# Kernel tuning notes

Measured on AMD Instinct MI355X. Metric: run time of the kernel, lower is better.

The kernel has to match this reference:

```python
import jax, jax.numpy as jnp
import numpy as np

# Transformer_E (depth=1): Residual(PreNorm(MultiScaleRetention)) + Residual1(PreNorm1(FeedForward))
# MultiScaleRetention follows the standard RetNet parallel form, adapted to two inputs
# (Q from x, K/V from z) as implied by PreNorm passing both normed streams to fn.

B, S, DIM, HEADS, MLP = 16, 1024, 256, 4, 512
HEAD = DIM // HEADS  # per-head qkv size; v_dim = DIM
EPS = 1e-5           # torch LayerNorm/GroupNorm default eps


def _ln(x, w, b):
    mu = jnp.mean(x, -1, keepdims=True)
    var = jnp.mean((x - mu) ** 2, -1, keepdims=True)
    return (x - mu) * jax.lax.rsqrt(var + EPS) * w + b


def _decay_matrix():
    # RetNet gammas: 1 - exp(linspace(log(1/32), log(1/512), heads))
    gammas = 1.0 - jnp.exp(jnp.linspace(jnp.log(1.0 / 32.0), jnp.log(1.0 / 512.0), HEADS))
    n = jnp.arange(S)
    diff = (n[:, None] - n[None, :]).astype(jnp.float32)  # [S,S]
    causal = diff >= 0
    D = jnp.where(causal[None], gammas[:, None, None] ** diff[None], 0.0)  # [H,S,S]
    return D.astype(jnp.float32)


def setup_inputs() -> dict:
    key = jax.random.key(0)
    ks = jax.random.split(key, 9)
    s = 1.0 / DIM  # repo inits W as randn/hidden_size
    return {
        "x": jax.random.normal(ks[0], (B, S, DIM), jnp.float32),
        "y": jax.random.normal(ks[1], (B, S, DIM), jnp.float32),
        "ln1_w": jnp.ones((DIM,), jnp.float32),
        "ln1_b": jnp.zeros((DIM,), jnp.float32),
        "W_Q": jax.random.normal(ks[2], (HEADS, DIM, HEAD), jnp.float32) * s,
        "W_K": jax.random.normal(ks[3], (HEADS, DIM, HEAD), jnp.float32) * s,
        "W_V": jax.random.normal(ks[4], (HEADS, DIM, HEAD), jnp.float32) * s,
        "gn_w": jnp.ones((DIM,), jnp.float32),
        "gn_b": jnp.zeros((DIM,), jnp.float32),
        "W_G": jax.random.normal(ks[5], (DIM, DIM), jnp.float32) * s,
        "W_O": jax.random.normal(ks[6], (DIM, DIM), jnp.float32) * s,
        "ln2_w": jnp.ones((DIM,), jnp.float32),
        "ln2_b": jnp.zeros((DIM,), jnp.float32),
        "ff_w1": jax.random.normal(ks[7], (DIM, MLP), jnp.float32) * (DIM ** -0.5),
        "ff_b1": jnp.zeros((MLP,), jnp.float32),
        "ff_w2": jax.random.normal(ks[8], (MLP, DIM), jnp.float32) * (MLP ** -0.5),
        "ff_b2": jnp.zeros((DIM,), jnp.float32),
    }


def reference(x, y, ln1_w, ln1_b, W_Q, W_K, W_V, gn_w, gn_b, W_G, W_O,
              ln2_w, ln2_b, ff_w1, ff_b1, ff_w2, ff_b2):
    # PreNorm: x.real -> float (already real float32 here), shared LayerNorm on both streams
    xn = _ln(x, ln1_w, ln1_b)
    zn = _ln(y, ln1_w, ln1_b)

    # --- MultiScaleRetention (parallel form) ---
    Q = jnp.einsum('bsd,hde->bhse', xn, W_Q)
    K = jnp.einsum('bsd,hde->bhse', zn, W_K)
    V = jnp.einsum('bsd,hde->bhse', zn, W_V)
    D = _decay_matrix()                                       # [H,S,S] causal decay
    scores = jnp.einsum('bhne,bhme->bhnm', Q, K) * D[None]    # [B,H,S,S]
    Yh = jnp.einsum('bhnm,bhme->bhne', scores, V)             # [B,H,S,HEAD]

    # GroupNorm(heads, v_dim) applied token-wise: normalize each head slice
    mu = jnp.mean(Yh, -1, keepdims=True)
    var = jnp.mean((Yh - mu) ** 2, -1, keepdims=True)
    Yn = (Yh - mu) * jax.lax.rsqrt(var + EPS)
    Ycat = jnp.transpose(Yn, (0, 2, 1, 3)).reshape(x.shape[0], x.shape[1], DIM)
    Ycat = Ycat * gn_w + gn_b

    # swish gate + output projection
    g = xn @ W_G
    attn_out = ((g * jax.nn.sigmoid(g)) * Ycat) @ W_O

    x1 = attn_out + x                                         # Residual

    # --- FeedForward block (Residual1(PreNorm1(FFN))) ---
    x1n = _ln(x1, ln2_w, ln2_b)
    h = jax.nn.leaky_relu(x1n @ ff_w1 + ff_b1, negative_slope=0.01)
    ff = h @ ff_w2 + ff_b2
    return ff + x1
```

## Files before the change

kernel.cpp:

```cpp
#include <hip/hip_runtime.h>

typedef float f32x4 __attribute__((ext_vector_type(4)));
typedef short bf16x8 __attribute__((ext_vector_type(8)));

__device__ __forceinline__ unsigned short f2bf(float f) {
  unsigned int u = __builtin_bit_cast(unsigned int, f);
  u += 0x7fffu + ((u >> 16) & 1u);
  return (unsigned short)(u >> 16);
}
__device__ __forceinline__ float bf2f(unsigned short s) {
  unsigned int u = ((unsigned int)s) << 16;
  return __builtin_bit_cast(float, u);
}

__device__ __forceinline__ void gll16(const void* src, void* dst) {
  __builtin_amdgcn_global_load_lds((const __attribute__((address_space(1))) void*)src,
                                   (__attribute__((address_space(3))) void*)dst, 16, 0, 0);
}

__global__ __launch_bounds__(256) void prep(
    const float* __restrict__ x, const float* __restrict__ y,
    const float* __restrict__ ln1w, const float* __restrict__ ln1b,
    const float* __restrict__ WQ, const float* __restrict__ WK,
    const float* __restrict__ WV, const float* __restrict__ WG,
    const float* __restrict__ WO, const float* __restrict__ F1,
    const float* __restrict__ F2,
    unsigned short* __restrict__ XN, unsigned short* __restrict__ ZN,
    unsigned short* __restrict__ qg, unsigned short* __restrict__ kv,
    unsigned short* __restrict__ wo, unsigned short* __restrict__ f1,
    unsigned short* __restrict__ f2)
{
  const int id = blockIdx.x;
  if (id < 8192) {
    const float* X = (id < 4096) ? x : y;
    unsigned short* Y = (id < 4096) ? XN : ZN;
    const int bid = id & 4095;
    const int lane = threadIdx.x & 63;
    const size_t row = (size_t)bid * 4 + (threadIdx.x >> 6);
    const float4 v = *reinterpret_cast<const float4*>(X + row * 256 + lane * 4);
    float s = v.x + v.y + v.z + v.w;
    #pragma unroll
    for (int off = 1; off < 64; off <<= 1) s += __shfl_xor(s, off);
    float mean = s * (1.0f / 256.0f);
    float dx = v.x - mean, dy = v.y - mean, dz = v.z - mean, dw = v.w - mean;
    float q = dx * dx + dy * dy + dz * dz + dw * dw;
    #pragma unroll
    for (int off = 1; off < 64; off <<= 1) q += __shfl_xor(q, off);
    float rstd = rsqrtf(q * (1.0f / 256.0f) + 1e-5f);
    float4 wv = *reinterpret_cast<const float4*>(ln1w + lane * 4);
    float4 bv = *reinterpret_cast<const float4*>(ln1b + lane * 4);
    ushort4 o;
    o.x = f2bf(dx * rstd * wv.x + bv.x);
    o.y = f2bf(dy * rstd * wv.y + bv.y);
    o.z = f2bf(dz * rstd * wv.z + bv.z);
    o.w = f2bf(dw * rstd * wv.w + bv.w);
    *reinterpret_cast<ushort4*>(Y + row * 256 + lane * 4) = o;
    return;
  }
  int i = (id - 8192) * 256 + threadIdx.x;
  if (i < 131072) {
    int n = i >> 8, d = i & 255;
    float v = (n < 256) ? WQ[((n >> 6) * 256 + d) * 64 + (n & 63)]
                        : WG[d * 256 + (n - 256)];
    qg[i] = f2bf(v);
  } else if (i < 262144) {
    int j = i - 131072; int n = j >> 8, d = j & 255;
    float v = (n < 256) ? WK[((n >> 6) * 256 + d) * 64 + (n & 63)]
                        : WV[(((n - 256) >> 6) * 256 + d) * 64 + ((n - 256) & 63)];
    kv[j] = f2bf(v);
  } else if (i < 327680) {
    int j = i - 262144; int n = j >> 8, d = j & 255;
    wo[j] = f2bf(WO[d * 256 + n]);
  } else if (i < 458752) {
    int j = i - 327680; int n = j >> 8, d = j & 255;
    f1[j] = f2bf(F1[d * 512 + n]);
  } else if (i < 589824) {
    int j = i - 458752; int n = j >> 9, k = j & 511;
    f2[j] = f2bf(F2[k * 256 + n]);
  }
}

__global__ __launch_bounds__(256) void gemm_qkvg(
    const unsigned short* __restrict__ XN, const unsigned short* __restrict__ ZN,
    const unsigned short* __restrict__ WQG, const unsigned short* __restrict__ WKV,
    unsigned short* __restrict__ QB, unsigned short* __restrict__ GB,
    unsigned short* __restrict__ KB, unsigned short* __restrict__ VT)
{
  __shared__ __align__(16) char sA[2][16384];
  __shared__ __align__(16) char sB[2][8192];
  const int tid = threadIdx.x, lane = tid & 63, w = tid >> 6;
  const int z = blockIdx.z;
  const unsigned short* A = z ? ZN : XN;
  const unsigned short* Bw = z ? WKV : WQG;
  const int flat = blockIdx.x + 8 * blockIdx.y;
  const int c = flat & 7, jj = flat >> 3;
  const int m0 = (c * 16 + (jj & 15)) * 128;
  const int n0 = (jj >> 4) * 64;
  const int wr = (w >> 1) * 64, wc = (w & 1) * 32;
  const char* Ab = (const char*)A + (size_t)m0 * 512;
  const char* Bb = (const char*)Bw + (size_t)n0 * 512;
  const int srow = lane >> 3;
  const int soff = 16 * ((lane & 7) ^ srow);
  f32x4 acc[4][2] = {};

  auto stage = [&](int bufi, int kt) {
    #pragma unroll
    for (int p = 0; p < 4; ++p) {
      int row = p * 32 + w * 8 + srow;
      gll16(Ab + (size_t)row * 512 + kt + soff, &sA[bufi][p * 4096 + w * 1024]);
    }
    #pragma unroll
    for (int p = 0; p < 2; ++p) {
      int row = p * 32 + w * 8 + srow;
      gll16(Bb + (size_t)row * 512 + kt + soff, &sB[bufi][p * 4096 + w * 1024]);
    }
  };

  stage(0, 0);
  asm volatile("s_waitcnt vmcnt(0)" ::: "memory");
  __syncthreads();
  int buf = 0;
  for (int kt = 0; kt < 512; kt += 128) {
    if (kt + 128 < 512) stage(buf ^ 1, kt + 128);
    #pragma unroll
    for (int kk = 0; kk < 2; ++kk) {
      const int ib = kk * 64 + ((lane >> 4) * 16);
      bf16x8 af[4], bfr[2];
      #pragma unroll
      for (int rf = 0; rf < 4; ++rf) {
        int row = wr + rf * 16 + (lane & 15);
        af[rf] = *reinterpret_cast<const bf16x8*>(&sA[buf][row * 128 + (ib ^ ((row & 7) << 4))]);
      }
      #pragma unroll
      for (int cf = 0; cf < 2; ++cf) {
        int row = wc + cf * 16 + (lane & 15);
        bfr[cf] = *reinterpret_cast<const bf16x8*>(&sB[buf][row * 128 + (ib ^ ((row & 7) << 4))]);
      }
      #pragma unroll
      for (int rf = 0; rf < 4; ++rf)
        #pragma unroll
        for (int cf = 0; cf < 2; ++cf)
          acc[rf][cf] = __builtin_amdgcn_mfma_f32_16x16x32_bf16(af[rf], bfr[cf], acc[rf][cf], 0, 0, 0);
    }
    asm volatile("s_waitcnt vmcnt(0)" ::: "memory");
    __syncthreads();
    buf ^= 1;
  }

  #pragma unroll
  for (int rf = 0; rf < 4; ++rf) {
    #pragma unroll
    for (int cf = 0; cf < 2; ++cf) {
      const int r0 = m0 + wr + rf * 16 + ((lane >> 4) * 4);
      const int col = n0 + wc + cf * 16 + (lane & 15);
      f32x4 v = acc[rf][cf];
      if (z == 0) {
        unsigned short* dst = (n0 < 256) ? QB : GB;
        int ccol = col & 255;
        #pragma unroll
        for (int j = 0; j < 4; ++j) dst[(size_t)(r0 + j) * 256 + ccol] = f2bf(v[j]);
      } else {
        if (n0 < 256) {
          #pragma unroll
          for (int j = 0; j < 4; ++j) KB[(size_t)(r0 + j) * 256 + col] = f2bf(v[j]);
        } else {
          int vc = col - 256, hh = vc >> 6, e = vc & 63;
          int bh = (r0 >> 10) * 4 + hh, s0 = r0 & 1023;
          ushort4 pk;
          pk.x = f2bf(v[0]); pk.y = f2bf(v[1]); pk.z = f2bf(v[2]); pk.w = f2bf(v[3]);
          *reinterpret_cast<ushort4*>(VT + (((size_t)bh * 64 + e) << 10) + s0) = pk;
        }
      }
    }
  }
}

template<int EPI>
__global__ __launch_bounds__(256) void gemm_nt(
    const unsigned short* __restrict__ A, const unsigned short* __restrict__ Bw,
    int K, unsigned short* __restrict__ o0,
    const float* __restrict__ bias, const float* __restrict__ resid,
    float* __restrict__ of)
{
  __shared__ __align__(16) char sA[2][16384];
  __shared__ __align__(16) char sB[2][8192];
  const int tid = threadIdx.x, lane = tid & 63, w = tid >> 6;
  const int flat = blockIdx.x + gridDim.x * blockIdx.y;
  const int c = flat & 7, jj = flat >> 3;
  const int m0 = (c * 16 + (jj & 15)) * 128;
  const int n0 = (jj >> 4) * 64;
  const int wr = (w >> 1) * 64, wc = (w & 1) * 32;
  const int K2 = K * 2;
  const char* Ab = (const char*)A + (size_t)m0 * K2;
  const char* Bb = (const char*)Bw + (size_t)n0 * K2;
  const int srow = lane >> 3;
  const int soff = 16 * ((lane & 7) ^ srow);
  f32x4 acc[4][2] = {};

  auto stage = [&](int bufi, int kt) {
    #pragma unroll
    for (int p = 0; p < 4; ++p) {
      int row = p * 32 + w * 8 + srow;
      gll16(Ab + (size_t)row * K2 + kt + soff, &sA[bufi][p * 4096 + w * 1024]);
    }
    #pragma unroll
    for (int p = 0; p < 2; ++p) {
      int row = p * 32 + w * 8 + srow;
      gll16(Bb + (size_t)row * K2 + kt + soff, &sB[bufi][p * 4096 + w * 1024]);
    }
  };

  stage(0, 0);
  asm volatile("s_waitcnt vmcnt(0)" ::: "memory");
  __syncthreads();
  int buf = 0;
  for (int kt = 0; kt < K2; kt += 128) {
    if (kt + 128 < K2) stage(buf ^ 1, kt + 128);
    #pragma unroll
    for (int kk = 0; kk < 2; ++kk) {
      const int ib = kk * 64 + ((lane >> 4) * 16);
      bf16x8 af[4], bfr[2];
      #pragma unroll
      for (int rf = 0; rf < 4; ++rf) {
        int row = wr + rf * 16 + (lane & 15);
        af[rf] = *reinterpret_cast<const bf16x8*>(&sA[buf][row * 128 + (ib ^ ((row & 7) << 4))]);
      }
      #pragma unroll
      for (int cf = 0; cf < 2; ++cf) {
        int row = wc + cf * 16 + (lane & 15);
        bfr[cf] = *reinterpret_cast<const bf16x8*>(&sB[buf][row * 128 + (ib ^ ((row & 7) << 4))]);
      }
      #pragma unroll
      for (int rf = 0; rf < 4; ++rf)
        #pragma unroll
        for (int cf = 0; cf < 2; ++cf)
          acc[rf][cf] = __builtin_amdgcn_mfma_f32_16x16x32_bf16(af[rf], bfr[cf], acc[rf][cf], 0, 0, 0);
    }
    asm volatile("s_waitcnt vmcnt(0)" ::: "memory");
    __syncthreads();
    buf ^= 1;
  }

  #pragma unroll
  for (int rf = 0; rf < 4; ++rf) {
    #pragma unroll
    for (int cf = 0; cf < 2; ++cf) {
      const int r0 = m0 + wr + rf * 16 + ((lane >> 4) * 4);
      const int col = n0 + wc + cf * 16 + (lane & 15);
      f32x4 v = acc[rf][cf];
      if constexpr (EPI == 3) {
        float bc = bias[col];
        #pragma unroll
        for (int j = 0; j < 4; ++j) {
          float t = v[j] + bc;
          o0[(size_t)(r0 + j) * 512 + col] = f2bf(t >= 0.0f ? t : 0.01f * t);
        }
      } else {
        float bc = bias[col];
        #pragma unroll
        for (int j = 0; j < 4; ++j) {
          size_t idx = (size_t)(r0 + j) * 256 + col;
          of[idx] = v[j] + bc + resid[idx];
        }
      }
    }
  }
}

__global__ __launch_bounds__(256) void gemm_wo_ln(
    const unsigned short* __restrict__ AY, const unsigned short* __restrict__ WoT,
    const float* __restrict__ x, const float* __restrict__ ln2w,
    const float* __restrict__ ln2b,
    float* __restrict__ X1, unsigned short* __restrict__ X1N)
{
  __shared__ __align__(16) char sA[2][4096];
  __shared__ __align__(16) char sB[2][32768];
  __shared__ float redS[32][4], redQ[32][4];
  const int tid = threadIdx.x, lane = tid & 63, w = tid >> 6;
  const int id = blockIdx.x;
  const int c = id & 7, j5 = id >> 3;
  const int m0 = (c * 64 + j5) * 32;
  const char* Ab = (const char*)AY + (size_t)m0 * 512;
  const char* Bb = (const char*)WoT;
  const int srow = lane >> 3;
  const int soff = 16 * ((lane & 7) ^ srow);
  f32x4 acc[2][4] = {};

  auto stage = [&](int bufi, int kt) {
    {
      int row = w * 8 + srow;
      gll16(Ab + (size_t)row * 512 + kt + soff, &sA[bufi][w * 1024]);
    }
    #pragma unroll
    for (int p = 0; p < 8; ++p) {
      int row = w * 64 + p * 8 + srow;
      gll16(Bb + (size_t)row * 512 + kt + soff, &sB[bufi][w * 8192 + p * 1024]);
    }
  };

  stage(0, 0);
  asm volatile("s_waitcnt vmcnt(0)" ::: "memory");
  __syncthreads();
  int buf = 0;
  for (int kt = 0; kt < 512; kt += 128) {
    if (kt + 128 < 512) stage(buf ^ 1, kt + 128);
    #pragma unroll
    for (int kk = 0; kk < 2; ++kk) {
      const int ib = kk * 64 + ((lane >> 4) * 16);
      bf16x8 af[2], bfr[4];
      #pragma unroll
      for (int mf = 0; mf < 2; ++mf) {
        int row = mf * 16 + (lane & 15);
        af[mf] = *reinterpret_cast<const bf16x8*>(&sA[buf][row * 128 + (ib ^ ((row & 7) << 4))]);
      }
      #pragma unroll
      for (int nf = 0; nf < 4; ++nf) {
        int row = w * 64 + nf * 16 + (lane & 15);
        bfr[nf] = *reinterpret_cast<const bf16x8*>(&sB[buf][row * 128 + (ib ^ ((row & 7) << 4))]);
      }
      #pragma unroll
      for (int mf = 0; mf < 2; ++mf)
        #pragma unroll
        for (int nf = 0; nf < 4; ++nf)
          acc[mf][nf] = __builtin_amdgcn_mfma_f32_16x16x32_bf16(af[mf], bfr[nf], acc[mf][nf], 0, 0, 0);
    }
    asm volatile("s_waitcnt vmcnt(0)" ::: "memory");
    __syncthreads();
    buf ^= 1;
  }

  #pragma unroll
  for (int mf = 0; mf < 2; ++mf) {
    #pragma unroll
    for (int j = 0; j < 4; ++j) {
      const int rowg = m0 + mf * 16 + ((lane >> 4) * 4) + j;
      float s = 0.0f, q = 0.0f;
      #pragma unroll
      for (int nf = 0; nf < 4; ++nf) {
        const int col = w * 64 + nf * 16 + (lane & 15);
        float v = acc[mf][nf][j] + x[(size_t)rowg * 256 + col];
        acc[mf][nf][j] = v;
        s += v; q += v * v;
      }
      #pragma unroll
      for (int off = 1; off < 16; off <<= 1) { s += __shfl_xor(s, off); q += __shfl_xor(q, off); }
      if ((lane & 15) == 0) {
        int rl = mf * 16 + ((lane >> 4) * 4) + j;
        redS[rl][w] = s; redQ[rl][w] = q;
      }
    }
  }
  __syncthreads();
  #pragma unroll
  for (int mf = 0; mf < 2; ++mf) {
    #pragma unroll
    for (int j = 0; j < 4; ++j) {
      const int rl = mf * 16 + ((lane >> 4) * 4) + j;
      const int rowg = m0 + rl;
      float sm = redS[rl][0] + redS[rl][1] + redS[rl][2] + redS[rl][3];
      float sq = redQ[rl][0] + redQ[rl][1] + redQ[rl][2] + redQ[rl][3];
      float mean = sm * (1.0f / 256.0f);
      float var = sq * (1.0f / 256.0f) - mean * mean;
      float rstd = rsqrtf(var + 1e-5f);
      #pragma unroll
      for (int nf = 0; nf < 4; ++nf) {
        const int col = w * 64 + nf * 16 + (lane & 15);
        float v = acc[mf][nf][j];
        X1[(size_t)rowg * 256 + col] = v;
        X1N[(size_t)rowg * 256 + col] = f2bf((v - mean) * rstd * ln2w[col] + ln2b[col]);
      }
    }
  }
}

__global__ __launch_bounds__(256) void attn_ret(
    const unsigned short* __restrict__ Qb, const unsigned short* __restrict__ Kb,
    const unsigned short* __restrict__ Vt, const unsigned short* __restrict__ Gb,
    const float* __restrict__ gnw, const float* __restrict__ gnb,
    unsigned short* __restrict__ AY)
{
  __shared__ __align__(16) char sK[2][8192];
  __shared__ __align__(16) char sV[2][8192];
  __shared__ __align__(16) char sP[8192];
  const int tid = threadIdx.x, lane = tid & 63, w = tid >> 6;
  const int id = blockIdx.x;
  const int c = id & 7, jid = id >> 3;
  const int bh = c * 8 + (jid & 7);
  const int g = jid >> 3;
  const int qt = (g < 4) ? (15 - g) : (g < 8) ? (11 - g) : (g < 12) ? g : (g - 12);
  const int b = bh >> 2, h = bh & 3;

  const float la = logf(1.0f / 32.0f), lb = logf(1.0f / 512.0f);
  const float gamma = 1.0f - expf(la + (lb - la) * ((float)h * (1.0f / 3.0f)));
  const float lg = log2f(gamma);

  const char* Qg = (const char*)Qb
      + ((size_t)(b * 1024 + qt * 64 + w * 16 + (lane & 15))) * 512 + h * 128 + (lane >> 4) * 16;
  const bf16x8 aq0 = *reinterpret_cast<const bf16x8*>(Qg);
  const bf16x8 aq1 = *reinterpret_cast<const bf16x8*>(Qg + 64);

  const int nloc_b = w * 16 + ((lane >> 4) * 4);
  float Aj[4], Bcf[4];
  #pragma unroll
  for (int j = 0; j < 4; ++j) Aj[j] = exp2f((float)(qt * 64 + nloc_b + j) * lg);
  #pragma unroll
  for (int cf = 0; cf < 4; ++cf) Bcf[cf] = exp2f(-(float)(cf * 16 + (lane & 15)) * lg);
  const float g64 = exp2f(-64.0f * lg);

  const char* Kg = (const char*)Kb + ((size_t)(b * 1024)) * 512 + h * 128;
  const char* Vg = (const char*)Vt + ((size_t)bh * 64) * 2048;
  const int srow = lane >> 3;
  const int soff = 16 * ((lane & 7) ^ srow);

  auto stage = [&](int bufi, int t) {
    const char* kb = Kg + (size_t)(t * 64) * 512;
    const char* vb = Vg + (size_t)(t * 64) * 2;
    #pragma unroll
    for (int p = 0; p < 2; ++p) {
      int row = p * 32 + w * 8 + srow;
      gll16(kb + (size_t)row * 512 + soff, &sK[bufi][p * 4096 + w * 1024]);
      gll16(vb + (size_t)row * 2048 + soff, &sV[bufi][p * 4096 + w * 1024]);
    }
  };

  stage(0, 0);
  f32x4 o[4] = {};
  asm volatile("s_waitcnt vmcnt(0)" ::: "memory");
  __syncthreads();
  int buf = 0;

  for (int t = 0; t <= qt; ++t) {
    if (t < qt) stage(buf ^ 1, t + 1);

    f32x4 s4[4] = {};
    #pragma unroll
    for (int kk = 0; kk < 2; ++kk) {
      const int ib = kk * 64 + ((lane >> 4) * 16);
      const bf16x8 aq = kk ? aq1 : aq0;
      #pragma unroll
      for (int cf = 0; cf < 4; ++cf) {
        int kr = cf * 16 + (lane & 15);
        bf16x8 bk = *reinterpret_cast<const bf16x8*>(&sK[buf][kr * 128 + (ib ^ ((kr & 7) << 4))]);
        s4[cf] = __builtin_amdgcn_mfma_f32_16x16x32_bf16(aq, bk, s4[cf], 0, 0, 0);
      }
    }

    const bool diag = (t == qt);
    #pragma unroll
    for (int cf = 0; cf < 4; ++cf) {
      const int mloc = cf * 16 + (lane & 15);
      #pragma unroll
      for (int j = 0; j < 4; ++j) {
        float p = s4[cf][j] * (Aj[j] * Bcf[cf]);
        if (diag && (nloc_b + j - mloc) < 0) p = 0.0f;
        int pr = nloc_b + j;
        *reinterpret_cast<unsigned short*>(sP + pr * 128 + ((mloc * 2) ^ ((pr & 7) << 4))) = f2bf(p);
      }
    }

    #pragma unroll
    for (int kk = 0; kk < 2; ++kk) {
      const int ib = kk * 64 + ((lane >> 4) * 16);
      int pr = w * 16 + (lane & 15);
      bf16x8 ap = *reinterpret_cast<const bf16x8*>(sP + pr * 128 + (ib ^ ((pr & 7) << 4)));
      #pragma unroll
      for (int cf = 0; cf < 4; ++cf) {
        int vr = cf * 16 + (lane & 15);
        bf16x8 bv = *reinterpret_cast<const bf16x8*>(&sV[buf][vr * 128 + (ib ^ ((vr & 7) << 4))]);
        o[cf] = __builtin_amdgcn_mfma_f32_16x16x32_bf16(ap, bv, o[cf], 0, 0, 0);
      }
    }
    #pragma unroll
    for (int j = 0; j < 4; ++j) Aj[j] *= g64;

    asm volatile("s_waitcnt vmcnt(0)" ::: "memory");
    __syncthreads();
    buf ^= 1;
  }

  float gw[4], gb[4];
  #pragma unroll
  for (int cf = 0; cf < 4; ++cf) {
    int col = h * 64 + cf * 16 + (lane & 15);
    gw[cf] = gnw[col]; gb[cf] = gnb[col];
  }
  const int tokb = b * 1024 + qt * 64 + nloc_b;
  #pragma unroll
  for (int j = 0; j < 4; ++j) {
    float sm = 0.0f, sq = 0.0f;
    #pragma unroll
    for (int cf = 0; cf < 4; ++cf) { float xv = o[cf][j]; sm += xv; sq += xv * xv; }
    #pragma unroll
    for (int off = 1; off < 16; off <<= 1) { sm += __shfl_xor(sm, off); sq += __shfl_xor(sq, off); }
    float mean = sm * (1.0f / 64.0f);
    float var = sq * (1.0f / 64.0f) - mean * mean;
    float rstd = rsqrtf(var + 1e-5f);
    size_t tok = (size_t)(tokb + j);
    #pragma unroll
    for (int cf = 0; cf < 4; ++cf) {
      int col = h * 64 + cf * 16 + (lane & 15);
      float yn = (o[cf][j] - mean) * rstd * gw[cf] + gb[cf];
      float gv = bf2f(Gb[tok * 256 + col]);
      float sg = gv / (1.0f + expf(-gv));
      AY[tok * 256 + col] = f2bf(yn * sg);
    }
  }
}

extern "C" void kernel_launch(void* const* d_in, const int* in_sizes, int n_in,
                              void* d_out, int out_size, void* d_ws, size_t ws_size,
                              hipStream_t stream) {
  const float* x     = (const float*)d_in[0];
  const float* y     = (const float*)d_in[1];
  const float* ln1_w = (const float*)d_in[2];
  const float* ln1_b = (const float*)d_in[3];
  const float* W_Q   = (const float*)d_in[4];
  const float* W_K   = (const float*)d_in[5];
  const float* W_V   = (const float*)d_in[6];
  const float* gn_w  = (const float*)d_in[7];
  const float* gn_b  = (const float*)d_in[8];
  const float* W_G   = (const float*)d_in[9];
  const float* W_O   = (const float*)d_in[10];
  const float* ln2_w = (const float*)d_in[11];
  const float* ln2_b = (const float*)d_in[12];
  const float* ff_w1 = (const float*)d_in[13];
  const float* ff_b1 = (const float*)d_in[14];
  const float* ff_w2 = (const float*)d_in[15];
  const float* ff_b2 = (const float*)d_in[16];

  char* ws = (char*)d_ws;
  const size_t MB = 1048576;
  unsigned short* XN  = (unsigned short*)(ws + 0 * MB);
  unsigned short* ZN  = (unsigned short*)(ws + 8 * MB);
  unsigned short* QB  = (unsigned short*)(ws + 16 * MB);
  unsigned short* KB  = (unsigned short*)(ws + 24 * MB);
  unsigned short* VT  = (unsigned short*)(ws + 32 * MB);
  unsigned short* GB  = (unsigned short*)(ws + 40 * MB);
  unsigned short* WQG = (unsigned short*)(ws + 48 * MB);
  unsigned short* WKV = (unsigned short*)(ws + 48 * MB + 262144);
  unsigned short* WOp = (unsigned short*)(ws + 48 * MB + 524288);
  unsigned short* F1p = (unsigned short*)(ws + 48 * MB + 655360);
  unsigned short* F2p = (unsigned short*)(ws + 48 * MB + 917504);
  float*          X1  = (float*)(ws + 16 * MB);
  unsigned short* X1N = (unsigned short*)(ws + 32 * MB);
  unsigned short* H   = (unsigned short*)(ws + 0 * MB);
  unsigned short* AY  = ZN;
  float* out = (float*)d_out;

  prep<<<10496, 256, 0, stream>>>(x, y, ln1_w, ln1_b, W_Q, W_K, W_V, W_G, W_O,
                                  ff_w1, ff_w2, XN, ZN, WQG, WKV, WOp, F1p, F2p);
  gemm_qkvg<<<dim3(8, 128, 2), 256, 0, stream>>>(XN, ZN, WQG, WKV, QB, GB, KB, VT);
  attn_ret<<<1024, 256, 0, stream>>>(QB, KB, VT, GB, gn_w, gn_b, AY);
  gemm_wo_ln<<<512, 256, 0, stream>>>(AY, WOp, x, ln2_w, ln2_b, X1, X1N);
  gemm_nt<3><<<dim3(8, 128), 256, 0, stream>>>(X1N, F1p, 256, H, ff_b1, nullptr, nullptr);
  gemm_nt<4><<<dim3(4, 128), 256, 0, stream>>>(H, F2p, 512, nullptr, ff_b2, X1, out);
}
```

Measured before the change: 100.5 us.

## Switch retention to chunkwise form with per-chunk KV state summaries

Replaces the quadratic parallel retention loop over all prior key tiles with a chunkwise-recurrent form. The QKV GEMM now also writes a decay-scaled, transposed K. A new kernel computes per-chunk K^T V state matrices in fp32. The attention kernel sums the decayed prior states and applies them with one extra MFMA, plus an intra-chunk diagonal block. This removes the O(S^2) inner loop and its load imbalance, at the cost of an extra launch, extra global traffic for the state matrices, a serial per-block accumulation over up to 15 states, and bf16 rounding of the decayed state.

```diff
diff --git a/kernel.cpp b/kernel.cpp
--- a/kernel.cpp
+++ b/kernel.cpp
@@ -2,6 +2,7 @@
 
 typedef float f32x4 __attribute__((ext_vector_type(4)));
 typedef short bf16x8 __attribute__((ext_vector_type(8)));
+typedef short s16x8 __attribute__((ext_vector_type(8)));
 
 __device__ __forceinline__ unsigned short f2bf(float f) {
   unsigned int u = __builtin_bit_cast(unsigned int, f);
@@ -84,7 +85,8 @@
     const unsigned short* __restrict__ XN, const unsigned short* __restrict__ ZN,
     const unsigned short* __restrict__ WQG, const unsigned short* __restrict__ WKV,
     unsigned short* __restrict__ QB, unsigned short* __restrict__ GB,
-    unsigned short* __restrict__ KB, unsigned short* __restrict__ VT)
+    unsigned short* __restrict__ KB, unsigned short* __restrict__ VT,
+    unsigned short* __restrict__ KTS)
 {
   __shared__ __align__(16) char sA[2][16384];
   __shared__ __align__(16) char sB[2][8192];
@@ -147,6 +149,7 @@
     buf ^= 1;
   }
 
+  const float la = logf(1.0f / 32.0f), lb = logf(1.0f / 512.0f);
   #pragma unroll
   for (int rf = 0; rf < 4; ++rf) {
     #pragma unroll
@@ -163,6 +166,19 @@
         if (n0 < 256) {
           #pragma unroll
           for (int j = 0; j < 4; ++j) KB[(size_t)(r0 + j) * 256 + col] = f2bf(v[j]);
+          int hh2 = col >> 6, kd = col & 63;
+          float gam = 1.0f - expf(la + (lb - la) * ((float)hh2 * (1.0f / 3.0f)));
+          float lgh = log2f(gam);
+          int tokc = r0 & 63;
+          float scl = exp2f(lgh * (float)(64 - tokc));
+          float gstep = exp2f(-lgh);
+          ushort4 ks;
+          ks.x = f2bf(v[0] * scl); scl *= gstep;
+          ks.y = f2bf(v[1] * scl); scl *= gstep;
+          ks.z = f2bf(v[2] * scl); scl *= gstep;
+          ks.w = f2bf(v[3] * scl);
+          int bh2 = (r0 >> 10) * 4 + hh2;
+          *reinterpret_cast<ushort4*>(KTS + ((size_t)bh2 * 64 + kd) * 1024 + (r0 & 1023)) = ks;
         } else {
           int vc = col - 256, hh = vc >> 6, e = vc & 63;
           int bh = (r0 >> 10) * 4 + hh, s0 = r0 & 1023;
@@ -373,21 +389,57 @@
   }
 }
 
-__global__ __launch_bounds__(256) void attn_ret(
-    const unsigned short* __restrict__ Qb, const unsigned short* __restrict__ Kb,
-    const unsigned short* __restrict__ Vt, const unsigned short* __restrict__ Gb,
-    const float* __restrict__ gnw, const float* __restrict__ gnb,
-    unsigned short* __restrict__ AY)
+__global__ __launch_bounds__(256) void calc_u(
+    const unsigned short* __restrict__ KTS, const unsigned short* __restrict__ VT,
+    float* __restrict__ UT)
 {
-  __shared__ __align__(16) char sK[2][8192];
-  __shared__ __align__(16) char sV[2][8192];
-  __shared__ __align__(16) char sP[8192];
   const int tid = threadIdx.x, lane = tid & 63, w = tid >> 6;
   const int id = blockIdx.x;
   const int c = id & 7, jid = id >> 3;
   const int bh = c * 8 + (jid & 7);
-  const int g = jid >> 3;
-  const int qt = (g < 4) ? (15 - g) : (g < 8) ? (11 - g) : (g < 12) ? g : (g - 12);
+  const int t = jid >> 3;
+
+  const char* Ka = (const char*)KTS +
+      (((size_t)bh * 64 + w * 16 + (lane & 15)) * 1024 + t * 64 + (lane >> 4) * 8) * 2;
+  const bf16x8 a0 = *reinterpret_cast<const bf16x8*>(Ka);
+  const bf16x8 a1 = *reinterpret_cast<const bf16x8*>(Ka + 64);
+
+  f32x4 c4[4] = {};
+  #pragma unroll
+  for (int kk = 0; kk < 2; ++kk) {
+    const bf16x8 a = kk ? a1 : a0;
+    #pragma unroll
+    for (int cf = 0; cf < 4; ++cf) {
+      const char* Vb = (const char*)VT +
+          (((size_t)bh * 64 + cf * 16 + (lane & 15)) * 1024 + t * 64 + kk * 32 + (lane >> 4) * 8) * 2;
+      bf16x8 bv = *reinterpret_cast<const bf16x8*>(Vb);
+      c4[cf] = __builtin_amdgcn_mfma_f32_16x16x32_bf16(a, bv, c4[cf], 0, 0, 0);
+    }
+  }
+  float* ub = UT + ((size_t)bh * 16 + t) * 4096;
+  #pragma unroll
+  for (int cf = 0; cf < 4; ++cf) {
+    int e = cf * 16 + (lane & 15);
+    *reinterpret_cast<f32x4*>(ub + e * 64 + w * 16 + (lane >> 4) * 4) = c4[cf];
+  }
+}
+
+__global__ __launch_bounds__(256) void attn_ret2(
+    const unsigned short* __restrict__ Qb, const unsigned short* __restrict__ Kb,
+    const unsigned short* __restrict__ Vt, const unsigned short* __restrict__ Gb,
+    const float* __restrict__ UT,
+    const float* __restrict__ gnw, const float* __restrict__ gnb,
+    unsigned short* __restrict__ AY)
+{
+  __shared__ __align__(16) char sK[8192];
+  __shared__ __align__(16) char sV[8192];
+  __shared__ __align__(16) char sP[8192];
+  __shared__ __align__(16) char sS[8192];
+  const int tid = threadIdx.x, lane = tid & 63, w = tid >> 6;
+  const int id = blockIdx.x;
+  const int c = id & 7, jid = id >> 3;
+  const int bh = c * 8 + (jid & 7);
+  const int qt = jid >> 3;
   const int b = bh >> 2, h = bh & 3;
 
   const float la = logf(1.0f / 32.0f), lb = logf(1.0f / 512.0f);
@@ -402,80 +454,106 @@
   const int nloc_b = w * 16 + ((lane >> 4) * 4);
   float Aj[4], Bcf[4];
   #pragma unroll
-  for (int j = 0; j < 4; ++j) Aj[j] = exp2f((float)(qt * 64 + nloc_b + j) * lg);
+  for (int j = 0; j < 4; ++j) Aj[j] = exp2f((float)(nloc_b + j) * lg);
   #pragma unroll
   for (int cf = 0; cf < 4; ++cf) Bcf[cf] = exp2f(-(float)(cf * 16 + (lane & 15)) * lg);
-  const float g64 = exp2f(-64.0f * lg);
-
-  const char* Kg = (const char*)Kb + ((size_t)(b * 1024)) * 512 + h * 128;
-  const char* Vg = (const char*)Vt + ((size_t)bh * 64) * 2048;
-  const int srow = lane >> 3;
-  const int soff = 16 * ((lane & 7) ^ srow);
-
-  auto stage = [&](int bufi, int t) {
-    const char* kb = Kg + (size_t)(t * 64) * 512;
-    const char* vb = Vg + (size_t)(t * 64) * 2;
+
+  {
+    const char* kb = (const char*)Kb + ((size_t)(b * 1024 + qt * 64)) * 512 + h * 128;
+    const char* vb = (const char*)Vt + ((size_t)bh * 64) * 2048 + (size_t)(qt * 64) * 2;
+    const int srow = lane >> 3;
+    const int soff = 16 * ((lane & 7) ^ srow);
     #pragma unroll
     for (int p = 0; p < 2; ++p) {
       int row = p * 32 + w * 8 + srow;
-      gll16(kb + (size_t)row * 512 + soff, &sK[bufi][p * 4096 + w * 1024]);
-      gll16(vb + (size_t)row * 2048 + soff, &sV[bufi][p * 4096 + w * 1024]);
-    }
-  };
-
-  stage(0, 0);
-  f32x4 o[4] = {};
+      gll16(kb + (size_t)row * 512 + soff, &sK[p * 4096 + w * 1024]);
+      gll16(vb + (size_t)row * 2048 + soff, &sV[p * 4096 + w * 1024]);
+    }
+  }
+
+  if (qt > 0) {
+    f32x4 sacc[4] = {};
+    float wgt = 1.0f;
+    const float g64c = exp2f(64.0f * lg);
+    const float* Ub = UT + ((size_t)bh * 16) * 4096;
+    for (int tp = qt - 1; tp >= 0; --tp) {
+      const f32x4* up = reinterpret_cast<const f32x4*>(Ub + (size_t)tp * 4096) + tid * 4;
+      #pragma unroll
+      for (int q = 0; q < 4; ++q) sacc[q] += up[q] * wgt;
+      wgt *= g64c;
+    }
+    const int e = tid >> 2, kb2 = (tid & 3) * 16;
+    s16x8 pk0, pk1;
+    #pragma unroll
+    for (int q = 0; q < 4; ++q) {
+      pk0[q]     = (short)f2bf(sacc[0][q]);
+      pk0[4 + q] = (short)f2bf(sacc[1][q]);
+      pk1[q]     = (short)f2bf(sacc[2][q]);
+      pk1[4 + q] = (short)f2bf(sacc[3][q]);
+    }
+    *reinterpret_cast<s16x8*>(sS + e * 128 + ((kb2 * 2) ^ ((e & 7) << 4))) = pk0;
+    *reinterpret_cast<s16x8*>(sS + e * 128 + ((kb2 * 2 + 16) ^ ((e & 7) << 4))) = pk1;
+  }
+
   asm volatile("s_waitcnt vmcnt(0)" ::: "memory");
   __syncthreads();
-  int buf = 0;
-
-  for (int t = 0; t <= qt; ++t) {
-    if (t < qt) stage(buf ^ 1, t + 1);
-
-    f32x4 s4[4] = {};
+
+  f32x4 s4[4] = {};
+  #pragma unroll
+  for (int kk = 0; kk < 2; ++kk) {
+    const int ib = kk * 64 + ((lane >> 4) * 16);
+    const bf16x8 aq = kk ? aq1 : aq0;
+    #pragma unroll
+    for (int cf = 0; cf < 4; ++cf) {
+      int kr = cf * 16 + (lane & 15);
+      bf16x8 bk = *reinterpret_cast<const bf16x8*>(&sK[kr * 128 + (ib ^ ((kr & 7) << 4))]);
+      s4[cf] = __builtin_amdgcn_mfma_f32_16x16x32_bf16(aq, bk, s4[cf], 0, 0, 0);
+    }
+  }
+
+  #pragma unroll
+  for (int cf = 0; cf < 4; ++cf) {
+    const int mloc = cf * 16 + (lane & 15);
+    #pragma unroll
+    for (int j = 0; j < 4; ++j) {
+      float p = s4[cf][j] * (Aj[j] * Bcf[cf]);
+      if ((nloc_b + j - mloc) < 0) p = 0.0f;
+      int pr = nloc_b + j;
+      *reinterpret_cast<unsigned short*>(sP + pr * 128 + ((mloc * 2) ^ ((pr & 7) << 4))) = f2bf(p);
+    }
+  }
+
+  f32x4 o[4] = {};
+  #pragma unroll
+  for (int kk = 0; kk < 2; ++kk) {
+    const int ib = kk * 64 + ((lane >> 4) * 16);
+    int pr = w * 16 + (lane & 15);
+    bf16x8 ap = *reinterpret_cast<const bf16x8*>(sP + pr * 128 + (ib ^ ((pr & 7) << 4)));
+    #pragma unroll
+    for (int cf = 0; cf < 4; ++cf) {
+      int vr = cf * 16 + (lane & 15);
+      bf16x8 bv = *reinterpret_cast<const bf16x8*>(&sV[vr * 128 + (ib ^ ((vr & 7) << 4))]);
+      o[cf] = __builtin_amdgcn_mfma_f32_16x16x32_bf16(ap, bv, o[cf], 0, 0, 0);
+    }
+  }
+
+  if (qt > 0) {
+    f32x4 ys[4] = {};
     #pragma unroll
     for (int kk = 0; kk < 2; ++kk) {
       const int ib = kk * 64 + ((lane >> 4) * 16);
       const bf16x8 aq = kk ? aq1 : aq0;
       #pragma unroll
       for (int cf = 0; cf < 4; ++cf) {
-        int kr = cf * 16 + (lane & 15);
-        bf16x8 bk = *reinterpret_cast<const bf16x8*>(&sK[buf][kr * 128 + (ib ^ ((kr & 7) << 4))]);
-        s4[cf] = __builtin_amdgcn_mfma_f32_16x16x32_bf16(aq, bk, s4[cf], 0, 0, 0);
-      }
-    }
-
-    const bool diag = (t == qt);
-    #pragma unroll
-    for (int cf = 0; cf < 4; ++cf) {
-      const int mloc = cf * 16 + (lane & 15);
-      #pragma unroll
-      for (int j = 0; j < 4; ++j) {
-        float p = s4[cf][j] * (Aj[j] * Bcf[cf]);
-        if (diag && (nloc_b + j - mloc) < 0) p = 0.0f;
-        int pr = nloc_b + j;
-        *reinterpret_cast<unsigned short*>(sP + pr * 128 + ((mloc * 2) ^ ((pr & 7) << 4))) = f2bf(p);
-      }
-    }
-
-    #pragma unroll
-    for (int kk = 0; kk < 2; ++kk) {
-      const int ib = kk * 64 + ((lane >> 4) * 16);
-      int pr = w * 16 + (lane & 15);
-      bf16x8 ap = *reinterpret_cast<const bf16x8*>(sP + pr * 128 + (ib ^ ((pr & 7) << 4)));
-      #pragma unroll
-      for (int cf = 0; cf < 4; ++cf) {
-        int vr = cf * 16 + (lane & 15);
-        bf16x8 bv = *reinterpret_cast<const bf16x8*>(&sV[buf][vr * 128 + (ib ^ ((vr & 7) << 4))]);
-        o[cf] = __builtin_amdgcn_mfma_f32_16x16x32_bf16(ap, bv, o[cf], 0, 0, 0);
-      }
-    }
-    #pragma unroll
-    for (int j = 0; j < 4; ++j) Aj[j] *= g64;
-
-    asm volatile("s_waitcnt vmcnt(0)" ::: "memory");
-    __syncthreads();
-    buf ^= 1;
+        int er = cf * 16 + (lane & 15);
+        bf16x8 bs = *reinterpret_cast<const bf16x8*>(&sS[er * 128 + (ib ^ ((er & 7) << 4))]);
+        ys[cf] = __builtin_amdgcn_mfma_f32_16x16x32_bf16(aq, bs, ys[cf], 0, 0, 0);
+      }
+    }
+    #pragma unroll
+    for (int cf = 0; cf < 4; ++cf)
+      #pragma unroll
+      for (int j = 0; j < 4; ++j) o[cf][j] += Aj[j] * ys[cf][j];
   }
 
   float gw[4], gb[4];
@@ -541,6 +619,8 @@
   unsigned short* WOp = (unsigned short*)(ws + 48 * MB + 524288);
   unsigned short* F1p = (unsigned short*)(ws + 48 * MB + 655360);
   unsigned short* F2p = (unsigned short*)(ws + 48 * MB + 917504);
+  unsigned short* KTS = (unsigned short*)(ws + 56 * MB);
+  float*          UT  = (float*)(ws + 64 * MB);
   float*          X1  = (float*)(ws + 16 * MB);
   unsigned short* X1N = (unsigned short*)(ws + 32 * MB);
   unsigned short* H   = (unsigned short*)(ws + 0 * MB);
@@ -549,8 +629,9 @@
 
   prep<<<10496, 256, 0, stream>>>(x, y, ln1_w, ln1_b, W_Q, W_K, W_V, W_G, W_O,
                                   ff_w1, ff_w2, XN, ZN, WQG, WKV, WOp, F1p, F2p);
-  gemm_qkvg<<<dim3(8, 128, 2), 256, 0, stream>>>(XN, ZN, WQG, WKV, QB, GB, KB, VT);
-  attn_ret<<<1024, 256, 0, stream>>>(QB, KB, VT, GB, gn_w, gn_b, AY);
+  gemm_qkvg<<<dim3(8, 128, 2), 256, 0, stream>>>(XN, ZN, WQG, WKV, QB, GB, KB, VT, KTS);
+  calc_u<<<1024, 256, 0, stream>>>(KTS, VT, UT);
+  attn_ret2<<<1024, 256, 0, stream>>>(QB, KB, VT, GB, UT, gn_w, gn_b, AY);
   gemm_wo_ln<<<512, 256, 0, stream>>>(AY, WOp, x, ln2_w, ln2_b, X1, X1N);
   gemm_nt<3><<<dim3(8, 128), 256, 0, stream>>>(X1N, F1p, 256, H, ff_b1, nullptr, nullptr);
   gemm_nt<4><<<dim3(4, 128), 256, 0, stream>>>(H, F2p, 512, nullptr, ff_b2, X1, out);
```

New measurement: 105.2 us. +4.7%, slower.
